# Kernel optimization log

Measured on AMD Instinct MI355X. Metric: run time of the kernel, lower is better.

The kernel has to match this reference:

```python
import jax, jax.numpy as jnp
import numpy as np

NUM_GRAPHS = 1024
NODES_PER_GRAPH = 1024
HIDDEN = 128
RANK_K = 8


def _mlp(x, w1, b1, w2, b2):
    # Linear -> ReLU -> Linear
    return jax.nn.relu(x @ w1 + b1) @ w2 + b2


def setup_inputs() -> dict:
    key = jax.random.key(0)
    ks = jax.random.split(key, 13)
    N = NUM_GRAPHS * NODES_PER_GRAPH
    H = jax.random.normal(ks[0], (N, HIDDEN), dtype=jnp.float32)
    # equal-size graphs: sorted graph ids 0..G-1, each repeated n_per times
    batch = jnp.repeat(jnp.arange(NUM_GRAPHS, dtype=jnp.int32), NODES_PER_GRAPH)
    s = 0.05
    p = {
        "d_w1": jax.random.normal(ks[1], (HIDDEN, HIDDEN)) * s,
        "d_b1": jnp.zeros((HIDDEN,), jnp.float32),
        "d_w2": jax.random.normal(ks[2], (HIDDEN, 2)) * s,
        "d_b2": jnp.zeros((2,), jnp.float32),
        "u_w1": jax.random.normal(ks[3], (HIDDEN, HIDDEN)) * s,
        "u_b1": jnp.zeros((HIDDEN,), jnp.float32),
        "u_w2": jax.random.normal(ks[4], (HIDDEN, 2 * RANK_K)) * s,
        "u_b2": jnp.zeros((2 * RANK_K,), jnp.float32),
        "s_w1": jax.random.normal(ks[5], (HIDDEN, HIDDEN)) * s,
        "s_b1": jnp.zeros((HIDDEN,), jnp.float32),
        "s_w2": jax.random.normal(ks[6], (HIDDEN, RANK_K)) * s,
        "s_b2": jnp.zeros((RANK_K,), jnp.float32),
    }
    return {"H": H, "batch": batch, **p}


def reference(H, batch, d_w1, d_b1, d_w2, d_b2, u_w1, u_b1, u_w2, u_b2, s_w1, s_b1, s_w2, s_b2):
    # per-node heads
    d_raw = _mlp(H, d_w1, d_b1, d_w2, d_b2)            # [N, 2]
    u_raw = _mlp(H, u_w1, u_b1, u_w2, u_b2)            # [N, 2k]
    # global_mean_pool: segment mean over graph ids
    sums = jax.ops.segment_sum(H, batch, num_segments=NUM_GRAPHS)          # [G, d]
    counts = jax.ops.segment_sum(jnp.ones((H.shape[0],), H.dtype), batch,
                                 num_segments=NUM_GRAPHS)                   # [G]
    h_pool = sums / counts[:, None]
    s_raw = _mlp(h_pool, s_w1, s_b1, s_w2, s_b2)       # [G, k]
    d_all = jax.nn.softplus(d_raw)
    s_all = jax.nn.softplus(s_raw)
    # equal-sized graphs -> the per-graph ragged gather+reshape is a pure reshape
    n = NODES_PER_GRAPH
    d = d_all.reshape(NUM_GRAPHS, 2 * n)               # per-graph d_g [2n]
    U = u_raw.reshape(NUM_GRAPHS, 2 * n, RANK_K)       # per-graph U_g [2n, k]
    return (d, U, s_all)
```

## Files before the change

### kernel.cpp

```cpp
#include <hip/hip_runtime.h>
#include <hip/hip_bf16.h>

#define G_NUM 1024
#define NPG   1024
#define HID   128
#define TILE_ROWS 32
#define TILES_PER_WG 64
#define GRAPHS_PER_WG 2

typedef __attribute__((ext_vector_type(8))) short   short8;
typedef __attribute__((ext_vector_type(4))) float   floatx4;

__device__ __forceinline__ unsigned short f2bf(float f) {
  unsigned int u = __float_as_uint(f);
  u += 0x7fffu + ((u >> 16) & 1u);
  return (unsigned short)(u >> 16);
}

__device__ __forceinline__ unsigned int cvt_pk_bf16(float lo, float hi) {
  unsigned int r;
  asm("v_cvt_pk_bf16_f32 %0, %1, %2" : "=v"(r) : "v"(lo), "v"(hi));
  return r;
}

__device__ __forceinline__ void wg_barrier_lds() {
  asm volatile("s_waitcnt lgkmcnt(0)\n\ts_barrier" ::: "memory");
}

__device__ __forceinline__ float softplusf(float x) {
  float t = exp2f(-fabsf(x) * 1.44269504f);
  return fmaxf(x, 0.f) + 0.69314718f * log2f(1.f + t);
}

__global__ void prep_kernel(const float* __restrict__ d_w1, const float* __restrict__ d_b1,
                            const float* __restrict__ d_w2,
                            const float* __restrict__ u_w1, const float* __restrict__ u_b1,
                            const float* __restrict__ u_w2,
                            const float* __restrict__ d_b2, const float* __restrict__ u_b2,
                            unsigned short* __restrict__ Wt1, unsigned short* __restrict__ W2t,
                            float* __restrict__ b1cat, float* __restrict__ b2cat)
{
  int id = blockIdx.x * blockDim.x + threadIdx.x;
  int stride = gridDim.x * blockDim.x;
  for (int idx = id; idx < 32768; idx += stride) {
    int c = idx >> 7, k = idx & 127;
    float v = (c < 128) ? d_w1[k * 128 + c] : u_w1[k * 128 + (c - 128)];
    Wt1[idx] = f2bf(v);
  }
  for (int idx = id; idx < 8192; idx += stride) {
    int c2 = idx >> 8, h = idx & 255;
    float v = 0.f;
    if (h < 128) { if (c2 < 2) v = d_w2[h * 2 + c2]; }
    else         { if (c2 >= 2 && c2 < 18) v = u_w2[(h - 128) * 16 + (c2 - 2)]; }
    W2t[idx] = f2bf(v);
  }
  for (int idx = id; idx < 256; idx += stride)
    b1cat[idx] = (idx < 128) ? d_b1[idx] : u_b1[idx - 128];
  for (int idx = id; idx < 32; idx += stride)
    b2cat[idx] = (idx < 2) ? d_b2[idx] : ((idx < 18) ? u_b2[idx - 2] : 0.f);
}

__global__ __launch_bounds__(256, 2) void fused_kernel(
    const float* __restrict__ H,
    const unsigned short* __restrict__ Wt1, const unsigned short* __restrict__ W2t,
    const float* __restrict__ b1cat, const float* __restrict__ b2cat,
    const float* __restrict__ s_w1, const float* __restrict__ s_b1,
    const float* __restrict__ s_w2, const float* __restrict__ s_b2,
    float* __restrict__ out)
{
  __shared__ __align__(16) unsigned short sH0 [TILE_ROWS * 128];
  __shared__ __align__(16) unsigned short sH1 [TILE_ROWS * 128];
  __shared__ __align__(16) unsigned short sC1a[TILE_ROWS * 256];
  __shared__ __align__(16) unsigned short sC1b[TILE_ROWS * 256];
  __shared__ __align__(16) float sX[768];

  const int tid  = threadIdx.x;
  const int g0   = blockIdx.x * GRAPHS_PER_WG;
  const int lane = tid & 63;
  const int w    = tid >> 6;
  const int l15  = lane & 15;
  const int l4   = lane >> 4;

  float* outD = out;
  float* outU = out + 2097152;
  float* outS = out + 18874368;

  short8 b1f[4][4];
  float  b1b[4];
#pragma unroll
  for (int nt = 0; nt < 4; ++nt) {
    int c = 64 * w + 16 * nt + l15;
    b1b[nt] = b1cat[c];
#pragma unroll
    for (int ks = 0; ks < 4; ++ks)
      b1f[nt][ks] = *(const short8*)(Wt1 + c * 128 + 32 * ks + 8 * l4);
  }
  const int r0 = 16 * (w >> 1);
  const int c0 = 16 * (w & 1);
  short8 w2f[8];
#pragma unroll
  for (int s8 = 0; s8 < 8; ++s8)
    w2f[s8] = *(const short8*)(W2t + (c0 + l15) * 256 + 32 * s8 + 8 * l4);
  const float b2v = b2cat[c0 + l15];

  const unsigned selw = (l15 & 1) ? 0x03020706u : 0x05040100u;
  const bool hi2 = (l15 & 2) != 0;

  const float* Hb = H + (long)g0 * (NPG * HID);

  float4 psum  = make_float4(0.f, 0.f, 0.f, 0.f);
  float4 pool0 = make_float4(0.f, 0.f, 0.f, 0.f);

  float4 svA[4], svB[4];
#pragma unroll
  for (int i = 0; i < 4; ++i) svA[i] = *(const float4*)(Hb + i * 1024 + tid * 4);
#pragma unroll
  for (int i = 0; i < 4; ++i) svB[i] = *(const float4*)(Hb + 4096 + i * 1024 + tid * 4);

  auto regionC = [&](const unsigned short* sCr, int tc) {
    floatx4 acc2 = {b2v, b2v, b2v, b2v};
#pragma unroll
    for (int s8 = 0; s8 < 8; ++s8) {
      int r = r0 + l15;
      int bo = r * 512 + 64 * s8 + 16 * l4;
      bo ^= (r & 7) << 4;
      short8 a2 = *(const short8*)((const char*)sCr + bo);
      acc2 = __builtin_amdgcn_mfma_f32_16x16x32_bf16(a2, w2f[s8], acc2, 0, 0, 0);
    }
    long nodebase = (long)g0 * NPG + tc * TILE_ROWS + r0 + 4 * l4;
    if (c0 == 0) {
#pragma unroll
      for (int q = 0; q < 4; ++q) {
        float v = acc2[q];
        long node = nodebase + q;
        if (l15 < 2) outD[node * 2 + l15] = softplusf(v);
        else         outU[node * 16 + (l15 - 2)] = v;
      }
    } else {
#pragma unroll
      for (int q = 0; q < 4; ++q) {
        long node = nodebase + q;
        if (l15 < 2) outU[node * 16 + 14 + l15] = acc2[q];
      }
    }
  };

  auto body = [&](float4 (&cur)[4], unsigned short* sHw,
                  const unsigned short* sCr, unsigned short* sCw, int t) {
#pragma unroll
    for (int i = 0; i < 4; ++i) {
      float4 v = cur[i];
      psum.x += v.x; psum.y += v.y; psum.z += v.z; psum.w += v.w;
      int row = i * 8 + (tid >> 5);
      int bo = row * 256 + (tid & 31) * 8;
      bo ^= (row & 7) << 4;
      uint2 p;
      p.x = cvt_pk_bf16(v.x, v.y);
      p.y = cvt_pk_bf16(v.z, v.w);
      *(uint2*)((char*)sHw + bo) = p;
    }
    if (t == 31) { pool0 = psum; psum = make_float4(0.f, 0.f, 0.f, 0.f); }
    if (t + 2 < TILES_PER_WG) {
      const float* nb = Hb + (t + 2) * (TILE_ROWS * HID);
#pragma unroll
      for (int i = 0; i < 4; ++i) cur[i] = *(const float4*)(nb + i * 1024 + tid * 4);
    }
    wg_barrier_lds();

    if (t > 0) regionC(sCr, t - 1);

    floatx4 acc[2][4];
#pragma unroll
    for (int mt = 0; mt < 2; ++mt)
#pragma unroll
      for (int nt = 0; nt < 4; ++nt)
        acc[mt][nt] = (floatx4){b1b[nt], b1b[nt], b1b[nt], b1b[nt]};

#pragma unroll
    for (int ks = 0; ks < 4; ++ks) {
      short8 a[2];
#pragma unroll
      for (int mt = 0; mt < 2; ++mt) {
        int row = 16 * mt + l15;
        int bo = row * 256 + 64 * ks + 16 * l4;
        bo ^= (row & 7) << 4;
        a[mt] = *(const short8*)((const char*)sHw + bo);
      }
#pragma unroll
      for (int mt = 0; mt < 2; ++mt)
#pragma unroll
        for (int nt = 0; nt < 4; ++nt)
          acc[mt][nt] = __builtin_amdgcn_mfma_f32_16x16x32_bf16(a[mt], b1f[nt][ks], acc[mt][nt], 0, 0, 0);
    }

#pragma unroll
    for (int mt = 0; mt < 2; ++mt) {
#pragma unroll
      for (int nt = 0; nt < 4; ++nt) {
        float v0 = fmaxf(acc[mt][nt][0], 0.f);
        float v1 = fmaxf(acc[mt][nt][1], 0.f);
        float v2 = fmaxf(acc[mt][nt][2], 0.f);
        float v3 = fmaxf(acc[mt][nt][3], 0.f);
        unsigned A = cvt_pk_bf16(v0, v1);
        unsigned B = cvt_pk_bf16(v2, v3);
        unsigned An = (unsigned)__builtin_amdgcn_mov_dpp((int)A, 0xB1, 0xF, 0xF, true);
        unsigned Bn = (unsigned)__builtin_amdgcn_mov_dpp((int)B, 0xB1, 0xF, 0xF, true);
        unsigned WA = __builtin_amdgcn_perm(An, A, selw);
        unsigned WB = __builtin_amdgcn_perm(Bn, B, selw);
        unsigned WAs = (unsigned)__builtin_amdgcn_mov_dpp((int)WA, 0x4E, 0xF, 0xF, true);
        unsigned WBs = (unsigned)__builtin_amdgcn_mov_dpp((int)WB, 0x4E, 0xF, 0xF, true);
        uint2 o;
        o.x = hi2 ? WBs : WA;
        o.y = hi2 ? WB  : WAs;
        int row = 16 * mt + 4 * l4 + (l15 & 3);
        int cb  = 64 * w + 16 * nt + (l15 & 12);
        int bo = row * 512 + cb * 2;
        bo ^= (row & 7) << 4;
        *(uint2*)((char*)sCw + bo) = o;
      }
    }
  };

  for (int t = 0; t < TILES_PER_WG; t += 2) {
    body(svA, sH0, sC1b, sC1a, t);
    body(svB, sH1, sC1a, sC1b, t + 1);
  }
  wg_barrier_lds();
  regionC(sC1b, TILES_PER_WG - 1);

  auto tail = [&](float4 p, int g) {
    __syncthreads();
    p.x += __shfl_xor(p.x, 32);
    p.y += __shfl_xor(p.y, 32);
    p.z += __shfl_xor(p.z, 32);
    p.w += __shfl_xor(p.w, 32);
    if (lane < 32) *(float4*)&sX[w * 128 + lane * 4] = p;
    __syncthreads();
    if (tid < 128) {
      float pc = sX[tid] + sX[128 + tid] + sX[256 + tid] + sX[384 + tid];
      sX[512 + tid] = pc;
    }
    __syncthreads();
    if (tid < 128) {
      float a = s_b1[tid];
      const float inv = 1.f / 1024.f;
#pragma unroll 8
      for (int k = 0; k < 128; ++k)
        a = fmaf(sX[512 + k] * inv, s_w1[k * 128 + tid], a);
      sX[640 + tid] = fmaxf(a, 0.f);
    }
    __syncthreads();
    if (tid < 8) {
      float a = s_b2[tid];
#pragma unroll 8
      for (int h = 0; h < 128; ++h)
        a = fmaf(sX[640 + h], s_w2[h * 8 + tid], a);
      outS[(long)g * 8 + tid] = softplusf(a);
    }
  };
  tail(pool0, g0);
  tail(psum,  g0 + 1);
}

extern "C" void kernel_launch(void* const* d_in, const int* in_sizes, int n_in,
                              void* d_out, int out_size, void* d_ws, size_t ws_size,
                              hipStream_t stream)
{
  const float* H    = (const float*)d_in[0];
  const float* d_w1 = (const float*)d_in[2];
  const float* d_b1 = (const float*)d_in[3];
  const float* d_w2 = (const float*)d_in[4];
  const float* d_b2 = (const float*)d_in[5];
  const float* u_w1 = (const float*)d_in[6];
  const float* u_b1 = (const float*)d_in[7];
  const float* u_w2 = (const float*)d_in[8];
  const float* u_b2 = (const float*)d_in[9];
  const float* s_w1 = (const float*)d_in[10];
  const float* s_b1 = (const float*)d_in[11];
  const float* s_w2 = (const float*)d_in[12];
  const float* s_b2 = (const float*)d_in[13];

  unsigned short* Wt1   = (unsigned short*)d_ws;
  unsigned short* W2t   = (unsigned short*)((char*)d_ws + 65536);
  float*          b1cat = (float*)((char*)d_ws + 81920);
  float*          b2cat = (float*)((char*)d_ws + 82944);

  hipLaunchKernelGGL(prep_kernel, dim3(64), dim3(256), 0, stream,
                     d_w1, d_b1, d_w2, u_w1, u_b1, u_w2, d_b2, u_b2,
                     Wt1, W2t, b1cat, b2cat);

  hipLaunchKernelGGL(fused_kernel, dim3(G_NUM / GRAPHS_PER_WG), dim3(256), 0, stream,
                     H, Wt1, W2t, b1cat, b2cat, s_w1, s_b1, s_w2, s_b2,
                     (float*)d_out);
}
```

Baseline: 152.9 us.

## Load MFMA A-fragments directly from global memory instead of staging H in LDS

Removes the sH0/sH1 LDS staging of the H tile. Each wave now reads its MFMA A operands straight from global memory (converting to bf16 in registers), while the coalesced prefetch is kept only for the pool sum and shrinks from two tiles ahead to one. The barrier moves to the end of each step, and the second-layer MFMA chain is split into two accumulators to shorten the dependency chain. s_setprio hints are added around the MFMA sections. This cuts LDS traffic and one barrier-related stall, but each tile of H is now read from global twice (once for the pool sum, once for the fragments), relying on the cache to absorb the second read. Latency hiding is also reduced.

```diff
diff --git a/kernel.cpp b/kernel.cpp
--- a/kernel.cpp
+++ b/kernel.cpp
@@ -68,8 +68,6 @@
     const float* __restrict__ s_w2, const float* __restrict__ s_b2,
     float* __restrict__ out)
 {
-  __shared__ __align__(16) unsigned short sH0 [TILE_ROWS * 128];
-  __shared__ __align__(16) unsigned short sH1 [TILE_ROWS * 128];
   __shared__ __align__(16) unsigned short sC1a[TILE_ROWS * 256];
   __shared__ __align__(16) unsigned short sC1b[TILE_ROWS * 256];
   __shared__ __align__(16) float sX[768];
@@ -111,27 +109,31 @@
   float4 psum  = make_float4(0.f, 0.f, 0.f, 0.f);
   float4 pool0 = make_float4(0.f, 0.f, 0.f, 0.f);
 
-  float4 svA[4], svB[4];
-#pragma unroll
-  for (int i = 0; i < 4; ++i) svA[i] = *(const float4*)(Hb + i * 1024 + tid * 4);
-#pragma unroll
-  for (int i = 0; i < 4; ++i) svB[i] = *(const float4*)(Hb + 4096 + i * 1024 + tid * 4);
+  float4 sv[4];
+#pragma unroll
+  for (int i = 0; i < 4; ++i) sv[i] = *(const float4*)(Hb + i * 1024 + tid * 4);
+
+  union U8 { unsigned int u[4]; short8 s; };
 
   auto regionC = [&](const unsigned short* sCr, int tc) {
-    floatx4 acc2 = {b2v, b2v, b2v, b2v};
+    floatx4 acc2a = {b2v, b2v, b2v, b2v};
+    floatx4 acc2b = {0.f, 0.f, 0.f, 0.f};
+    __builtin_amdgcn_s_setprio(1);
 #pragma unroll
     for (int s8 = 0; s8 < 8; ++s8) {
       int r = r0 + l15;
       int bo = r * 512 + 64 * s8 + 16 * l4;
       bo ^= (r & 7) << 4;
       short8 a2 = *(const short8*)((const char*)sCr + bo);
-      acc2 = __builtin_amdgcn_mfma_f32_16x16x32_bf16(a2, w2f[s8], acc2, 0, 0, 0);
-    }
+      if (s8 & 1) acc2b = __builtin_amdgcn_mfma_f32_16x16x32_bf16(a2, w2f[s8], acc2b, 0, 0, 0);
+      else        acc2a = __builtin_amdgcn_mfma_f32_16x16x32_bf16(a2, w2f[s8], acc2a, 0, 0, 0);
+    }
+    __builtin_amdgcn_s_setprio(0);
     long nodebase = (long)g0 * NPG + tc * TILE_ROWS + r0 + 4 * l4;
     if (c0 == 0) {
 #pragma unroll
       for (int q = 0; q < 4; ++q) {
-        float v = acc2[q];
+        float v = acc2a[q] + acc2b[q];
         long node = nodebase + q;
         if (l15 < 2) outD[node * 2 + l15] = softplusf(v);
         else         outU[node * 16 + (l15 - 2)] = v;
@@ -140,34 +142,45 @@
 #pragma unroll
       for (int q = 0; q < 4; ++q) {
         long node = nodebase + q;
-        if (l15 < 2) outU[node * 16 + 14 + l15] = acc2[q];
+        if (l15 < 2) outU[node * 16 + 14 + l15] = acc2a[q] + acc2b[q];
       }
     }
   };
 
-  auto body = [&](float4 (&cur)[4], unsigned short* sHw,
-                  const unsigned short* sCr, unsigned short* sCw, int t) {
-#pragma unroll
-    for (int i = 0; i < 4; ++i) {
-      float4 v = cur[i];
-      psum.x += v.x; psum.y += v.y; psum.z += v.z; psum.w += v.w;
-      int row = i * 8 + (tid >> 5);
-      int bo = row * 256 + (tid & 31) * 8;
-      bo ^= (row & 7) << 4;
-      uint2 p;
-      p.x = cvt_pk_bf16(v.x, v.y);
-      p.y = cvt_pk_bf16(v.z, v.w);
-      *(uint2*)((char*)sHw + bo) = p;
+  auto step = [&](int t, const unsigned short* sCr, unsigned short* sCw) {
+    {
+      float4 a0 = sv[0], a1 = sv[1], a2 = sv[2], a3 = sv[3];
+      psum.x += a0.x + a1.x + a2.x + a3.x;
+      psum.y += a0.y + a1.y + a2.y + a3.y;
+      psum.z += a0.z + a1.z + a2.z + a3.z;
+      psum.w += a0.w + a1.w + a2.w + a3.w;
     }
     if (t == 31) { pool0 = psum; psum = make_float4(0.f, 0.f, 0.f, 0.f); }
-    if (t + 2 < TILES_PER_WG) {
-      const float* nb = Hb + (t + 2) * (TILE_ROWS * HID);
-#pragma unroll
-      for (int i = 0; i < 4; ++i) cur[i] = *(const float4*)(nb + i * 1024 + tid * 4);
-    }
-    wg_barrier_lds();
+    if (t + 1 < TILES_PER_WG) {
+      const float* nb = Hb + (long)(t + 1) * (TILE_ROWS * HID);
+#pragma unroll
+      for (int i = 0; i < 4; ++i) sv[i] = *(const float4*)(nb + i * 1024 + tid * 4);
+    }
 
     if (t > 0) regionC(sCr, t - 1);
+
+    const float* tb = Hb + (long)t * (TILE_ROWS * HID);
+    short8 af[4][2];
+#pragma unroll
+    for (int ks = 0; ks < 4; ++ks) {
+#pragma unroll
+      for (int mt = 0; mt < 2; ++mt) {
+        const float* p = tb + (16 * mt + l15) * HID + 32 * ks + 8 * l4;
+        float4 f0 = *(const float4*)p;
+        float4 f1 = *(const float4*)(p + 4);
+        U8 u;
+        u.u[0] = cvt_pk_bf16(f0.x, f0.y);
+        u.u[1] = cvt_pk_bf16(f0.z, f0.w);
+        u.u[2] = cvt_pk_bf16(f1.x, f1.y);
+        u.u[3] = cvt_pk_bf16(f1.z, f1.w);
+        af[ks][mt] = u.s;
+      }
+    }
 
     floatx4 acc[2][4];
 #pragma unroll
@@ -176,22 +189,15 @@
       for (int nt = 0; nt < 4; ++nt)
         acc[mt][nt] = (floatx4){b1b[nt], b1b[nt], b1b[nt], b1b[nt]};
 
-#pragma unroll
-    for (int ks = 0; ks < 4; ++ks) {
-      short8 a[2];
-#pragma unroll
-      for (int mt = 0; mt < 2; ++mt) {
-        int row = 16 * mt + l15;
-        int bo = row * 256 + 64 * ks + 16 * l4;
-        bo ^= (row & 7) << 4;
-        a[mt] = *(const short8*)((const char*)sHw + bo);
-      }
+    __builtin_amdgcn_s_setprio(1);
+#pragma unroll
+    for (int ks = 0; ks < 4; ++ks)
 #pragma unroll
       for (int mt = 0; mt < 2; ++mt)
 #pragma unroll
         for (int nt = 0; nt < 4; ++nt)
-          acc[mt][nt] = __builtin_amdgcn_mfma_f32_16x16x32_bf16(a[mt], b1f[nt][ks], acc[mt][nt], 0, 0, 0);
-    }
+          acc[mt][nt] = __builtin_amdgcn_mfma_f32_16x16x32_bf16(af[ks][mt], b1f[nt][ks], acc[mt][nt], 0, 0, 0);
+    __builtin_amdgcn_s_setprio(0);
 
 #pragma unroll
     for (int mt = 0; mt < 2; ++mt) {
@@ -219,13 +225,13 @@
         *(uint2*)((char*)sCw + bo) = o;
       }
     }
+    wg_barrier_lds();
   };
 
   for (int t = 0; t < TILES_PER_WG; t += 2) {
-    body(svA, sH0, sC1b, sC1a, t);
-    body(svB, sH1, sC1a, sC1b, t + 1);
+    step(t,     sC1b, sC1a);
+    step(t + 1, sC1a, sC1b);
   }
-  wg_barrier_lds();
   regionC(sC1b, TILES_PER_WG - 1);
 
   auto tail = [&](float4 p, int g) {
```

After: 303.4 us. +98.5%, slower.
